# Kernel optimization log

Measured on AMD Instinct MI355X. Metric: run time of the kernel, lower is better.

The kernel has to match this reference:

```python
import jax, jax.numpy as jnp
import numpy as np


def _maxpool3d(x):
    # 3x3x3 max pool, stride 1, padding 1 (torch pads with -inf for max pool)
    return jax.lax.reduce_window(
        x, -jnp.inf, jax.lax.max,
        window_dimensions=(1, 1, 3, 3, 3),
        window_strides=(1, 1, 1, 1, 1),
        padding=[(0, 0), (0, 0), (1, 1), (1, 1), (1, 1)],
    )


def _soft_erode(x):
    return -_maxpool3d(-x)


def _soft_dilate(x):
    return _maxpool3d(x)


def _soft_open(x):
    return _soft_dilate(_soft_erode(x))


def setup_inputs() -> dict:
    key = jax.random.key(0)
    img = jax.random.uniform(key, (2, 1, 192, 256, 256), dtype=jnp.float32)
    return {"img": img}


def reference(img):
    # NOTE: in the original torch module, `skel` is computed via soft_close +
    # an iterative relu(skel - soft_open(skel)) loop, but the final line
    # `skel = F.relu(img - soft_open(img))` overwrites it entirely, so the
    # loop is dead code and the output depends only on img.
    opened = _soft_open(img)  # dilate(erode(img)), morphological opening
    return jax.nn.relu(img - opened)
```

## Files before the change

### kernel.cpp

```cpp
#include <hip/hip_runtime.h>
#include <math.h>


#define D_ 192
#define H_ 256
#define W_ 256
#define NB 2
#define TH 32
#define TW 64
#define CD 16
#define NCHUNK (D_ / CD)

#define RAW_H (TH + 4)
#define RAW_W (TW + 8)
#define RAW_S 76
#define EB_H  (TH + 2)
#define EB_W  (TW + 8)
#define EB_S  76

#define NRAWF4 (RAW_H * (RAW_W / 4))
#define NBTASK (EB_H * (EB_W / 8))

__device__ __forceinline__ float min3f(float a, float b, float c) {
    return fminf(fminf(a, b), c);
}
__device__ __forceinline__ float max3f(float a, float b, float c) {
    return fmaxf(fmaxf(a, b), c);
}

__global__ __launch_bounds__(256, 3)
void soft_skel_v7(const float* __restrict__ img, float* __restrict__ out) {
    __shared__ __align__(16) float raw[2][RAW_H][RAW_S];
    __shared__ __align__(16) float ebuf[2][EB_H][EB_S];

    const int tid  = threadIdx.x;
    const int lane = tid & 63;
    const int w0 = blockIdx.x * TW;
    const int h0 = blockIdx.y * TH;
    const int n  = blockIdx.z / NCHUNK;
    const int ch = blockIdx.z - n * NCHUNK;
    const int z0 = ch * CD;

    const float* vol  = img + (size_t)n * (D_ * H_ * W_);
    float*       ovol = out + (size_t)n * (D_ * H_ * W_);

    const float PINF = INFINITY;

    bool a_slot[3], a_img[3];
    int  a_lds[3], a_off[3];
    #pragma unroll
    for (int k = 0; k < 3; ++k) {
        int idx = tid + 256 * k;
        bool slot = idx < NRAWF4;
        int row = idx / (RAW_W / 4);
        int cg  = idx - row * (RAW_W / 4);
        int gh = h0 - 2 + row;
        int gw = w0 - 4 + 4 * cg;
        a_slot[k] = slot;
        a_img[k]  = slot && (gh >= 0) && (gh < H_) && (gw >= 0) && (gw <= W_ - 4);
        a_off[k]  = gh * W_ + gw;
        a_lds[k]  = slot ? (row * RAW_S + 4 * cg) : 0;
    }

    const int  r0 = tid / 9;
    const int  c0 = (tid - r0 * 9) * 8;
    const bool has1 = tid < (NBTASK - 256);
    const int  t1 = tid + 256;
    const int  r1 = t1 / 9;
    const int  c1 = (t1 - r1 * 9) * 8;

    const int ty = tid >> 3;
    const int cx = tid & 7;
    const int xx = cx * 8;

    float pm0[8], sp0[8], pm1[8], sp1[8];
    float t2A[8], t2B[8], t2C[8];
    float rw0[8], rw1[8], rw2[8];
    #pragma unroll
    for (int j = 0; j < 8; ++j) {
        pm0[j] = sp0[j] = pm1[j] = sp1[j] = PINF;
        t2A[j] = t2B[j] = 0.f;
        rw0[j] = rw1[j] = 0.f;
    }

    auto prefetch = [&](int zz, float4 L[3]) {
        const bool zok = (zz >= 0) && (zz < D_);
        const float* plane = vol + (size_t)zz * (H_ * W_);
        #pragma unroll
        for (int k = 0; k < 3; ++k) {
            float4 v = make_float4(PINF, PINF, PINF, PINF);
            if (zok && a_img[k]) v = *(const float4*)(plane + a_off[k]);
            L[k] = v;
        }
    };

    auto btask = [&](const float (*rb)[RAW_S], float (*eb)[EB_S],
                     int r, int cb, float pm[8], float sp[8], bool zeok) {
        float4 q00 = *(const float4*)(&rb[r][cb]);
        float4 q01 = *(const float4*)(&rb[r][cb + 4]);
        float4 q10 = *(const float4*)(&rb[r + 1][cb]);
        float4 q11 = *(const float4*)(&rb[r + 1][cb + 4]);
        float4 q20 = *(const float4*)(&rb[r + 2][cb]);
        float4 q21 = *(const float4*)(&rb[r + 2][cb + 4]);
        float v[8];
        v[0] = min3f(q00.x, q10.x, q20.x);
        v[1] = min3f(q00.y, q10.y, q20.y);
        v[2] = min3f(q00.z, q10.z, q20.z);
        v[3] = min3f(q00.w, q10.w, q20.w);
        v[4] = min3f(q01.x, q11.x, q21.x);
        v[5] = min3f(q01.y, q11.y, q21.y);
        v[6] = min3f(q01.z, q11.z, q21.z);
        v[7] = min3f(q01.w, q11.w, q21.w);

        float vL = __shfl_up(v[7], 1);
        float vR = __shfl_down(v[0], 1);
        if (lane == 0) {
            int cl = cb - 1; if (cl < 0) cl = 0;
            vL = min3f(rb[r][cl], rb[r + 1][cl], rb[r + 2][cl]);
        }
        if (lane == 63) {
            int cr = cb + 8; if (cr > RAW_W - 1) cr = RAW_W - 1;
            vR = min3f(rb[r][cr], rb[r + 1][cr], rb[r + 2][cr]);
        }

        float s[8];
        s[0] = min3f(vL, v[0], v[1]);
        #pragma unroll
        for (int j = 1; j < 7; ++j) s[j] = min3f(v[j - 1], v[j], v[j + 1]);
        s[7] = min3f(v[6], v[7], vR);

        const bool rok = zeok && ((unsigned)(h0 - 1 + r) < (unsigned)H_);
        float e[8];
        #pragma unroll
        for (int j = 0; j < 8; ++j) {
            float ev = fminf(pm[j], s[j]);
            bool ok = rok && ((unsigned)(w0 - 4 + cb + j) < (unsigned)W_);
            e[j] = ok ? ev : -PINF;
            pm[j] = fminf(sp[j], s[j]);
            sp[j] = s[j];
        }
        *(float4*)&eb[r][cb]     = make_float4(e[0], e[1], e[2], e[3]);
        *(float4*)&eb[r][cb + 4] = make_float4(e[4], e[5], e[6], e[7]);
    };

    float4 L[3];
    prefetch(z0 - 2, L);
    const int zzend = z0 + CD + 2;
    int cur = 0;

    for (int zz = z0 - 2; zz <= zzend; ++zz) {
        float (*rb)[RAW_S]        = raw[cur];
        const float (*rbp)[RAW_S] = raw[cur ^ 1];
        float (*eb)[EB_S]         = ebuf[cur];
        const float (*ebp)[EB_S]  = ebuf[cur ^ 1];

        #pragma unroll
        for (int k = 0; k < 3; ++k)
            if (a_slot[k]) *(float4*)(&rb[0][0] + a_lds[k]) = L[k];

        float4 c0v = *(const float4*)&rbp[ty + 2][xx + 4];
        float4 c1v = *(const float4*)&rbp[ty + 2][xx + 8];

        __syncthreads();

        if (zz < zzend) prefetch(zz + 1, L);

        rw2[0] = c0v.x; rw2[1] = c0v.y; rw2[2] = c0v.z; rw2[3] = c0v.w;
        rw2[4] = c1v.x; rw2[5] = c1v.y; rw2[6] = c1v.z; rw2[7] = c1v.w;

        const int  ze   = zz - 1;
        const bool zeok = (ze >= 0) && (ze < D_);
        btask(rb, eb, r0, c0, pm0, sp0, zeok);
        if (has1) btask(rb, eb, r1, c1, pm1, sp1, zeok);

        {
            const float* p0 = &ebp[ty][0];
            const float* p1 = &ebp[ty + 1][0];
            const float* p2 = &ebp[ty + 2][0];
            float4 q00 = *(const float4*)(p0 + xx + 4);
            float4 q01 = *(const float4*)(p0 + xx + 8);
            float4 q10 = *(const float4*)(p1 + xx + 4);
            float4 q11 = *(const float4*)(p1 + xx + 8);
            float4 q20 = *(const float4*)(p2 + xx + 4);
            float4 q21 = *(const float4*)(p2 + xx + 8);
            float t[8];
            t[0] = max3f(q00.x, q10.x, q20.x);
            t[1] = max3f(q00.y, q10.y, q20.y);
            t[2] = max3f(q00.z, q10.z, q20.z);
            t[3] = max3f(q00.w, q10.w, q20.w);
            t[4] = max3f(q01.x, q11.x, q21.x);
            t[5] = max3f(q01.y, q11.y, q21.y);
            t[6] = max3f(q01.z, q11.z, q21.z);
            t[7] = max3f(q01.w, q11.w, q21.w);

            float tL = __shfl_up(t[7], 1);
            float tR = __shfl_down(t[0], 1);
            if (cx == 0) {
                tL = max3f(p0[xx + 3], p1[xx + 3], p2[xx + 3]);
            }
            if (cx == 7) {
                tR = max3f(p0[xx + 12], p1[xx + 12], p2[xx + 12]);
            }
            t2C[0] = max3f(tL, t[0], t[1]);
            #pragma unroll
            for (int j = 1; j < 7; ++j) t2C[j] = max3f(t[j - 1], t[j], t[j + 1]);
            t2C[7] = max3f(t[6], t[7], tR);
        }

        if (zz >= z0 + 3) {
            const int z = zz - 3;
            float* op = ovol + ((size_t)z * H_ + (h0 + ty)) * W_ + (w0 + xx);
            float o[8];
            #pragma unroll
            for (int j = 0; j < 8; ++j) {
                float opened = max3f(t2A[j], t2B[j], t2C[j]);
                float v = rw0[j] - opened;
                o[j] = v > 0.f ? v : 0.f;
            }
            *(float4*)op       = make_float4(o[0], o[1], o[2], o[3]);
            *(float4*)(op + 4) = make_float4(o[4], o[5], o[6], o[7]);
        }

        #pragma unroll
        for (int j = 0; j < 8; ++j) {
            t2A[j] = t2B[j]; t2B[j] = t2C[j];
            rw0[j] = rw1[j]; rw1[j] = rw2[j];
        }
        cur ^= 1;
    }
}

extern "C" void kernel_launch(void* const* d_in, const int* in_sizes, int n_in,
                              void* d_out, int out_size, void* d_ws, size_t ws_size,
                              hipStream_t stream) {
    const float* img = (const float*)d_in[0];
    float* out = (float*)d_out;

    dim3 grid(W_ / TW, H_ / TH, NB * NCHUNK);
    dim3 block(256);
    soft_skel_v7<<<grid, block, 0, stream>>>(img, out);
}
```

Baseline: 194.0 us.

## Load erosion inputs directly from global memory, drop raw LDS staging buffer

Removes the shared-memory raw tile and its explicit register prefetch. Each erosion task now reads its 3-row, 8-column window straight from global memory, relying on L1/L2 to absorb the overlapping rows. The erosion buffer becomes triple-buffered so the erode and dilate phases can share one barrier per plane. This cuts LDS traffic and frees shared memory, but gives up the software prefetch overlap and adds redundant global loads plus an extra register pipeline stage.

```diff
diff --git a/kernel.cpp b/kernel.cpp
--- a/kernel.cpp
+++ b/kernel.cpp
@@ -11,14 +11,10 @@
 #define CD 16
 #define NCHUNK (D_ / CD)
 
-#define RAW_H (TH + 4)
-#define RAW_W (TW + 8)
-#define RAW_S 76
 #define EB_H  (TH + 2)
 #define EB_W  (TW + 8)
 #define EB_S  76
 
-#define NRAWF4 (RAW_H * (RAW_W / 4))
 #define NBTASK (EB_H * (EB_W / 8))
 
 __device__ __forceinline__ float min3f(float a, float b, float c) {
@@ -29,9 +25,8 @@
 }
 
 __global__ __launch_bounds__(256, 3)
-void soft_skel_v7(const float* __restrict__ img, float* __restrict__ out) {
-    __shared__ __align__(16) float raw[2][RAW_H][RAW_S];
-    __shared__ __align__(16) float ebuf[2][EB_H][EB_S];
+void soft_skel_v8(const float* __restrict__ img, float* __restrict__ out) {
+    __shared__ __align__(16) float ebuf[3][EB_H][EB_S];
 
     const int tid  = threadIdx.x;
     const int lane = tid & 63;
@@ -46,22 +41,6 @@
 
     const float PINF = INFINITY;
 
-    bool a_slot[3], a_img[3];
-    int  a_lds[3], a_off[3];
-    #pragma unroll
-    for (int k = 0; k < 3; ++k) {
-        int idx = tid + 256 * k;
-        bool slot = idx < NRAWF4;
-        int row = idx / (RAW_W / 4);
-        int cg  = idx - row * (RAW_W / 4);
-        int gh = h0 - 2 + row;
-        int gw = w0 - 4 + 4 * cg;
-        a_slot[k] = slot;
-        a_img[k]  = slot && (gh >= 0) && (gh < H_) && (gw >= 0) && (gw <= W_ - 4);
-        a_off[k]  = gh * W_ + gw;
-        a_lds[k]  = slot ? (row * RAW_S + 4 * cg) : 0;
-    }
-
     const int  r0 = tid / 9;
     const int  c0 = (tid - r0 * 9) * 8;
     const bool has1 = tid < (NBTASK - 256);
@@ -73,35 +52,56 @@
     const int cx = tid & 7;
     const int xx = cx * 8;
 
+    int  ro0[3], ro1[3];
+    bool rk0[3], rk1[3];
+    const int g0 = w0 - 4 + c0;
+    const int g1 = w0 - 4 + c1;
+    #pragma unroll
+    for (int i = 0; i < 3; ++i) {
+        int gh0 = h0 - 2 + r0 + i;
+        rk0[i] = (unsigned)gh0 < (unsigned)H_;
+        ro0[i] = gh0 * W_ + g0;
+        int gh1 = h0 - 2 + r1 + i;
+        rk1[i] = (unsigned)gh1 < (unsigned)H_;
+        ro1[i] = gh1 * W_ + g1;
+    }
+    const bool ck0a = (unsigned)g0       <= (unsigned)(W_ - 4);
+    const bool ck0b = (unsigned)(g0 + 4) <= (unsigned)(W_ - 4);
+    const bool ck1a = (unsigned)g1       <= (unsigned)(W_ - 4);
+    const bool ck1b = (unsigned)(g1 + 4) <= (unsigned)(W_ - 4);
+    const bool cl0 = (unsigned)(g0 - 1) < (unsigned)W_;
+    const bool cr0 = (unsigned)(g0 + 8) < (unsigned)W_;
+    const bool cl1 = (unsigned)(g1 - 1) < (unsigned)W_;
+    const bool cr1 = (unsigned)(g1 + 8) < (unsigned)W_;
+    const int coff = (h0 + ty) * W_ + (w0 + xx);
+
     float pm0[8], sp0[8], pm1[8], sp1[8];
     float t2A[8], t2B[8], t2C[8];
-    float rw0[8], rw1[8], rw2[8];
+    float rw0[8], rw1[8], rw2[8], rw3[8];
     #pragma unroll
     for (int j = 0; j < 8; ++j) {
         pm0[j] = sp0[j] = pm1[j] = sp1[j] = PINF;
         t2A[j] = t2B[j] = 0.f;
-        rw0[j] = rw1[j] = 0.f;
+        rw0[j] = rw1[j] = rw2[j] = 0.f;
     }
 
-    auto prefetch = [&](int zz, float4 L[3]) {
-        const bool zok = (zz >= 0) && (zz < D_);
-        const float* plane = vol + (size_t)zz * (H_ * W_);
-        #pragma unroll
-        for (int k = 0; k < 3; ++k) {
-            float4 v = make_float4(PINF, PINF, PINF, PINF);
-            if (zok && a_img[k]) v = *(const float4*)(plane + a_off[k]);
-            L[k] = v;
-        }
+    auto ld4 = [&](const float* p, bool ok) -> float4 {
+        return ok ? *(const float4*)p : make_float4(PINF, PINF, PINF, PINF);
     };
-
-    auto btask = [&](const float (*rb)[RAW_S], float (*eb)[EB_S],
-                     int r, int cb, float pm[8], float sp[8], bool zeok) {
-        float4 q00 = *(const float4*)(&rb[r][cb]);
-        float4 q01 = *(const float4*)(&rb[r][cb + 4]);
-        float4 q10 = *(const float4*)(&rb[r + 1][cb]);
-        float4 q11 = *(const float4*)(&rb[r + 1][cb + 4]);
-        float4 q20 = *(const float4*)(&rb[r + 2][cb]);
-        float4 q21 = *(const float4*)(&rb[r + 2][cb + 4]);
+    auto ld1 = [&](const float* p, bool ok) -> float {
+        return ok ? *p : PINF;
+    };
+
+    auto btask = [&](const float* pz, bool zokB, bool zeok, bool shfl_edges,
+                     int r, int cb, const int* ro, const bool* rk,
+                     bool cka, bool ckb, bool cl, bool cr,
+                     float* pm, float* sp, float (*ebw)[EB_S]) {
+        float4 q00 = ld4(pz + ro[0],     zokB && rk[0] && cka);
+        float4 q01 = ld4(pz + ro[0] + 4, zokB && rk[0] && ckb);
+        float4 q10 = ld4(pz + ro[1],     zokB && rk[1] && cka);
+        float4 q11 = ld4(pz + ro[1] + 4, zokB && rk[1] && ckb);
+        float4 q20 = ld4(pz + ro[2],     zokB && rk[2] && cka);
+        float4 q21 = ld4(pz + ro[2] + 4, zokB && rk[2] && ckb);
         float v[8];
         v[0] = min3f(q00.x, q10.x, q20.x);
         v[1] = min3f(q00.y, q10.y, q20.y);
@@ -112,15 +112,27 @@
         v[6] = min3f(q01.z, q11.z, q21.z);
         v[7] = min3f(q01.w, q11.w, q21.w);
 
-        float vL = __shfl_up(v[7], 1);
-        float vR = __shfl_down(v[0], 1);
-        if (lane == 0) {
-            int cl = cb - 1; if (cl < 0) cl = 0;
-            vL = min3f(rb[r][cl], rb[r + 1][cl], rb[r + 2][cl]);
-        }
-        if (lane == 63) {
-            int cr = cb + 8; if (cr > RAW_W - 1) cr = RAW_W - 1;
-            vR = min3f(rb[r][cr], rb[r + 1][cr], rb[r + 2][cr]);
+        float vL, vR;
+        if (shfl_edges) {
+            vL = __shfl_up(v[7], 1);
+            vR = __shfl_down(v[0], 1);
+            if (lane == 0) {
+                vL = min3f(ld1(pz + ro[0] - 1, zokB && rk[0] && cl),
+                           ld1(pz + ro[1] - 1, zokB && rk[1] && cl),
+                           ld1(pz + ro[2] - 1, zokB && rk[2] && cl));
+            }
+            if (lane == 63) {
+                vR = min3f(ld1(pz + ro[0] + 8, zokB && rk[0] && cr),
+                           ld1(pz + ro[1] + 8, zokB && rk[1] && cr),
+                           ld1(pz + ro[2] + 8, zokB && rk[2] && cr));
+            }
+        } else {
+            vL = min3f(ld1(pz + ro[0] - 1, zokB && rk[0] && cl),
+                       ld1(pz + ro[1] - 1, zokB && rk[1] && cl),
+                       ld1(pz + ro[2] - 1, zokB && rk[2] && cl));
+            vR = min3f(ld1(pz + ro[0] + 8, zokB && rk[0] && cr),
+                       ld1(pz + ro[1] + 8, zokB && rk[1] && cr),
+                       ld1(pz + ro[2] + 8, zokB && rk[2] && cr));
         }
 
         float s[8];
@@ -139,39 +151,34 @@
             pm[j] = fminf(sp[j], s[j]);
             sp[j] = s[j];
         }
-        *(float4*)&eb[r][cb]     = make_float4(e[0], e[1], e[2], e[3]);
-        *(float4*)&eb[r][cb + 4] = make_float4(e[4], e[5], e[6], e[7]);
+        *(float4*)&ebw[r][cb]     = make_float4(e[0], e[1], e[2], e[3]);
+        *(float4*)&ebw[r][cb + 4] = make_float4(e[4], e[5], e[6], e[7]);
     };
 
-    float4 L[3];
-    prefetch(z0 - 2, L);
+    int cur = 0;
     const int zzend = z0 + CD + 2;
-    int cur = 0;
 
     for (int zz = z0 - 2; zz <= zzend; ++zz) {
-        float (*rb)[RAW_S]        = raw[cur];
-        const float (*rbp)[RAW_S] = raw[cur ^ 1];
-        float (*eb)[EB_S]         = ebuf[cur];
-        const float (*ebp)[EB_S]  = ebuf[cur ^ 1];
-
-        #pragma unroll
-        for (int k = 0; k < 3; ++k)
-            if (a_slot[k]) *(float4*)(&rb[0][0] + a_lds[k]) = L[k];
-
-        float4 c0v = *(const float4*)&rbp[ty + 2][xx + 4];
-        float4 c1v = *(const float4*)&rbp[ty + 2][xx + 8];
+        const int prv = (cur == 0) ? 2 : cur - 1;
+        float (*ebw)[EB_S]       = ebuf[cur];
+        const float (*ebp)[EB_S] = ebuf[prv];
+        const float* pz = vol + (long long)zz * (H_ * W_);
+        const bool zokB = (zz >= 0) && (zz < D_) && (zz <= z0 + CD + 1);
+        const bool zeok = (zz - 1 >= 0) && (zz - 1 < D_);
+
+        float4 c0v = ld4(pz + coff,     zokB);
+        float4 c1v = ld4(pz + coff + 4, zokB);
+
+        btask(pz, zokB, zeok, true, r0, c0, ro0, rk0, ck0a, ck0b, cl0, cr0,
+              pm0, sp0, ebw);
+        if (has1)
+            btask(pz, zokB, zeok, true, r1, c1, ro1, rk1, ck1a, ck1b, cl1, cr1,
+                  pm1, sp1, ebw);
+
+        rw3[0] = c0v.x; rw3[1] = c0v.y; rw3[2] = c0v.z; rw3[3] = c0v.w;
+        rw3[4] = c1v.x; rw3[5] = c1v.y; rw3[6] = c1v.z; rw3[7] = c1v.w;
 
         __syncthreads();
-
-        if (zz < zzend) prefetch(zz + 1, L);
-
-        rw2[0] = c0v.x; rw2[1] = c0v.y; rw2[2] = c0v.z; rw2[3] = c0v.w;
-        rw2[4] = c1v.x; rw2[5] = c1v.y; rw2[6] = c1v.z; rw2[7] = c1v.w;
-
-        const int  ze   = zz - 1;
-        const bool zeok = (ze >= 0) && (ze < D_);
-        btask(rb, eb, r0, c0, pm0, sp0, zeok);
-        if (has1) btask(rb, eb, r1, c1, pm1, sp1, zeok);
 
         {
             const float* p0 = &ebp[ty][0];
@@ -224,9 +231,9 @@
         #pragma unroll
         for (int j = 0; j < 8; ++j) {
             t2A[j] = t2B[j]; t2B[j] = t2C[j];
-            rw0[j] = rw1[j]; rw1[j] = rw2[j];
-        }
-        cur ^= 1;
+            rw0[j] = rw1[j]; rw1[j] = rw2[j]; rw2[j] = rw3[j];
+        }
+        cur = (cur == 2) ? 0 : cur + 1;
     }
 }
 
@@ -238,5 +245,5 @@
 
     dim3 grid(W_ / TW, H_ / TH, NB * NCHUNK);
     dim3 block(256);
-    soft_skel_v7<<<grid, block, 0, stream>>>(img, out);
-}
+    soft_skel_v8<<<grid, block, 0, stream>>>(img, out);
+}
```

Measured after the change: 230.7 us. 1.19x slower.
